# Performance work log

Measured on AMD Instinct MI355X. Metric: run time of the kernel, lower is better.

The kernel has to match this reference:

```python
import jax, jax.numpy as jnp
import numpy as np

N, D_IN, D_OUT, N_CLASSES = 4096, 1024, 256, 64


def setup_inputs() -> dict:
    key = jax.random.key(0)
    k1, k2, k3, k4 = jax.random.split(key, 4)
    x = jax.random.normal(k1, (N, D_IN), dtype=jnp.float32)
    W = jax.random.normal(k2, (D_IN, D_OUT), dtype=jnp.float32) * 0.02
    b = jax.random.normal(k3, (D_OUT,), dtype=jnp.float32) * 0.02
    targets = jax.random.randint(k4, (N,), 0, N_CLASSES, dtype=jnp.int64)
    return {"x": x, "W": W, "b": b, "targets": targets}


def reference(x, W, b, targets):
    # FC projection (activation = 'linear')
    h = jnp.matmul(x, W) + b                      # [N, d]
    # Pairwise euclidean distances D[i, j] = ||h_i - h_j||_2, matching
    # tf.norm(tf.abs(anchor - others), axis=1) in the original per-anchor loop.
    sq = jnp.sum(h * h, axis=1)                   # [N]
    d2 = sq[:, None] + sq[None, :] - 2.0 * jnp.matmul(h, h.T)
    dist = jnp.sqrt(jnp.maximum(d2, 0.0))         # [N, N]
    same = targets[:, None] == targets[None, :]   # class_division mask
    inf = jnp.float32(np.inf)
    # Hardest positive: max distance among same-class (includes self at 0,
    hardest_pos = jnp.max(jnp.where(same, dist, -inf), axis=1)  # [N]
    # Hardest negative: min distance among different-class samples.
    hardest_neg = jnp.min(jnp.where(same, inf, dist), axis=1)   # [N]
    loss = jnp.sum(jnp.log1p(jnp.exp(hardest_pos - hardest_neg)))
    return loss
```

## Files before the change

kernel.cpp:

```cpp
#include <hip/hip_runtime.h>
#include <math.h>

#define NROWS 4096
#define DIN   1024
#define DOUT  256
#define NJB   64
#define NPAIR 528

using bfrag = __attribute__((ext_vector_type(8))) short;
using ffrag = __attribute__((ext_vector_type(4))) float;


static __device__ __forceinline__ unsigned short f2bf(float f) {
    unsigned int u = __float_as_uint(f);
    u = (u + 0x7fffu + ((u >> 16) & 1u)) >> 16;
    return (unsigned short)u;
}
static __device__ __forceinline__ unsigned int pack2(float lo, float hi) {
    return (unsigned int)f2bf(lo) | ((unsigned int)f2bf(hi) << 16);
}

__global__ __launch_bounds__(256) void setup(const float* __restrict__ x,
                                             const float* __restrict__ W,
                                             unsigned short* __restrict__ xs,
                                             unsigned short* __restrict__ Ws,
                                             float* __restrict__ sq,
                                             float* __restrict__ out) {
    const int f  = blockIdx.x * 256 + threadIdx.x;
    {
        const int l  = f & 63;
        const int ks = (f >> 6) & 31;
        const int t  = f >> 11;
        const int row = t * 16 + (l & 15);
        const int k0  = ks * 32 + (l >> 4) * 8;
        const float4 p0 = *(const float4*)&x[(size_t)row * DIN + k0];
        const float4 p1 = *(const float4*)&x[(size_t)row * DIN + k0 + 4];
        uint4 v;
        v.x = pack2(p0.x, p0.y);
        v.y = pack2(p0.z, p0.w);
        v.z = pack2(p1.x, p1.y);
        v.w = pack2(p1.z, p1.w);
        *(uint4*)&xs[(size_t)f * 8] = v;
    }
    if (f < 32768) {
        const int l  = f & 63;
        const int ks = (f >> 6) & 31;
        const int nt = f >> 11;
        const int col = nt * 16 + (l & 15);
        const int k0  = ks * 32 + (l >> 4) * 8;
        float a[8];
#pragma unroll
        for (int j = 0; j < 8; ++j) a[j] = W[(size_t)(k0 + j) * DOUT + col];
        uint4 v;
        v.x = pack2(a[0], a[1]);
        v.y = pack2(a[2], a[3]);
        v.z = pack2(a[4], a[5]);
        v.w = pack2(a[6], a[7]);
        *(uint4*)&Ws[(size_t)f * 8] = v;
    }
    if (f < NROWS) sq[f] = 0.0f;
    if (f == 0) *out = 0.0f;
}

__global__ __launch_bounds__(256) void gemm1_reg(
    const unsigned short* __restrict__ xs, const unsigned short* __restrict__ Ws,
    const float* __restrict__ b,
    unsigned short* __restrict__ hs, float* __restrict__ sq) {
    __shared__ __align__(16) short T[4][16][24];

    const int tid = threadIdx.x;
    const int w   = tid >> 6;
    const int l   = tid & 63;
    const int m16 = l & 15;
    const int q   = l >> 4;
    const int gw  = blockIdx.x * 4 + w;
    const int t   = gw >> 4;
    const int nt  = gw & 15;

    const bfrag* A = (const bfrag*)xs + ((size_t)t * 32) * 64 + l;
    const bfrag* B = (const bfrag*)Ws + ((size_t)nt * 32) * 64 + l;

    ffrag acc = {};
#pragma unroll
    for (int ks = 0; ks < 32; ++ks)
        acc = __builtin_amdgcn_mfma_f32_16x16x32_bf16(A[ks * 64], B[ks * 64], acc, 0, 0, 0);

    const float bc = b[nt * 16 + m16];
    float hv[4];
#pragma unroll
    for (int reg = 0; reg < 4; ++reg) hv[reg] = acc[reg] + bc;

#pragma unroll
    for (int reg = 0; reg < 4; ++reg) {
        float p = hv[reg] * hv[reg];
#pragma unroll
        for (int mask = 1; mask < 16; mask <<= 1) p += __shfl_xor(p, mask);
        if (m16 == 0) atomicAdd(&sq[t * 16 + q * 4 + reg], p);
    }

#pragma unroll
    for (int reg = 0; reg < 4; ++reg)
        T[w][q * 4 + reg][m16] = f2bf(hv[reg]);

    const int ksH  = nt >> 1;
    const int half = nt & 1;
    const int qp   = q - 2 * half;
    if (qp >= 0 && qp < 2) {
        bfrag v = *(const bfrag*)&T[w][m16][qp * 8];
        ((bfrag*)hs)[((size_t)t * 8 + ksH) * 64 + l] = v;
    }
}

__global__ __launch_bounds__(256) void hardest_tri(
    const unsigned short* __restrict__ hs, const float* __restrict__ sq,
    const int* __restrict__ targets,
    float* __restrict__ pmax, float* __restrict__ pmin) {
    const int tid = threadIdx.x;
    const int w   = tid >> 6;
    const int wi  = w & 1, wj = w >> 1;
    const int l   = tid & 63;
    const int m16 = l & 15;
    const int q   = l >> 4;

    const int k = blockIdx.x;
    int bj = (int)((sqrtf(8.0f * (float)k + 1.0f) - 1.0f) * 0.5f);
    while ((bj + 1) * (bj + 2) / 2 <= k) ++bj;
    while (bj * (bj + 1) / 2 > k) --bj;
    const int bi = k - bj * (bj + 1) / 2;
    const bool diag = (bi == bj);

    const int iw = bi * 128 + wi * 64;
    const int jw = bj * 128 + wj * 64;
    const int tA = iw >> 4;
    const int tB = jw >> 4;

    ffrag acc[4][4] = {};

#pragma unroll
    for (int ks = 0; ks < 8; ++ks) {
        bfrag a[4], bb[4];
#pragma unroll
        for (int mi = 0; mi < 4; ++mi)
            a[mi] = *(const bfrag*)&hs[(((size_t)(tA + mi) * 8 + ks) * 64 + l) * 8];
#pragma unroll
        for (int nj = 0; nj < 4; ++nj)
            bb[nj] = *(const bfrag*)&hs[(((size_t)(tB + nj) * 8 + ks) * 64 + l) * 8];
#pragma unroll
        for (int mi = 0; mi < 4; ++mi)
#pragma unroll
            for (int nj = 0; nj < 4; ++nj)
                acc[mi][nj] = __builtin_amdgcn_mfma_f32_16x16x32_bf16(
                    a[mi], bb[nj], acc[mi][nj], 0, 0, 0);
    }

    int   tj[4];
    float svj[4];
#pragma unroll
    for (int nj = 0; nj < 4; ++nj) {
        const int col = jw + nj * 16 + m16;
        tj[nj]  = targets[col];
        svj[nj] = sq[col];
    }

    float cmx[4], cmn[4];
#pragma unroll
    for (int nj = 0; nj < 4; ++nj) { cmx[nj] = -INFINITY; cmn[nj] = INFINITY; }

    const int jblk = bj * 2 + wj;
#pragma unroll
    for (int mi = 0; mi < 4; ++mi)
#pragma unroll
        for (int reg = 0; reg < 4; ++reg) {
            const int row = iw + mi * 16 + q * 4 + reg;
            const int ti  = targets[row];
            const float si = sq[row];
            float mx = -INFINITY, mn = INFINITY;
#pragma unroll
            for (int nj = 0; nj < 4; ++nj) {
                const float g    = acc[mi][nj][reg];
                const float vrow = fmaf(-2.0f, g, svj[nj]);
                const float vcol = fmaf(-2.0f, g, si);
                if (tj[nj] == ti) {
                    mx = fmaxf(mx, vrow);
                    cmx[nj] = fmaxf(cmx[nj], vcol);
                } else {
                    mn = fminf(mn, vrow);
                    cmn[nj] = fminf(cmn[nj], vcol);
                }
            }
#pragma unroll
            for (int mask = 1; mask < 16; mask <<= 1) {
                mx = fmaxf(mx, __shfl_xor(mx, mask));
                mn = fminf(mn, __shfl_xor(mn, mask));
            }
            if (m16 == 0) {
                pmax[(size_t)jblk * NROWS + row] = mx;
                pmin[(size_t)jblk * NROWS + row] = mn;
            }
        }

    if (!diag) {
        const int iblk = bi * 2 + wi;
#pragma unroll
        for (int nj = 0; nj < 4; ++nj) {
            float mx = cmx[nj], mn = cmn[nj];
            mx = fmaxf(mx, __shfl_xor(mx, 16));
            mn = fminf(mn, __shfl_xor(mn, 16));
            mx = fmaxf(mx, __shfl_xor(mx, 32));
            mn = fminf(mn, __shfl_xor(mn, 32));
            if (q == 0) {
                const int col = jw + nj * 16 + m16;
                pmax[(size_t)iblk * NROWS + col] = mx;
                pmin[(size_t)iblk * NROWS + col] = mn;
            }
        }
    }
}

__global__ __launch_bounds__(256) void finalize(const float* __restrict__ sq,
                                                const float* __restrict__ pmax,
                                                const float* __restrict__ pmin,
                                                float* __restrict__ out) {
    __shared__ float wsum[4];
    const int i = blockIdx.x * 256 + threadIdx.x;
    float mp = -INFINITY, mn = INFINITY;
#pragma unroll
    for (int c = 0; c < NJB; ++c) {
        mp = fmaxf(mp, pmax[c * NROWS + i]);
        mn = fminf(mn, pmin[c * NROWS + i]);
    }
    const float si = sq[i];
    const float hp = sqrtf(fmaxf(si + mp, 0.0f));
    const float hn = sqrtf(fmaxf(si + mn, 0.0f));
    const float d  = hp - hn;
    float li = fmaxf(d, 0.0f) + log1pf(expf(-fabsf(d)));
#pragma unroll
    for (int off = 32; off; off >>= 1) li += __shfl_down(li, off);
    const int lane = threadIdx.x & 63, wv = threadIdx.x >> 6;
    if (lane == 0) wsum[wv] = li;
    __syncthreads();
    if (threadIdx.x == 0)
        atomicAdd(out, wsum[0] + wsum[1] + wsum[2] + wsum[3]);
}

extern "C" void kernel_launch(void* const* d_in, const int* in_sizes, int n_in,
                              void* d_out, int out_size, void* d_ws, size_t ws_size,
                              hipStream_t stream) {
    const float* x       = (const float*)d_in[0];
    const float* W       = (const float*)d_in[1];
    const float* b       = (const float*)d_in[2];
    const int*   targets = (const int*)d_in[3];
    float* out = (float*)d_out;

    unsigned short* Ws   = (unsigned short*)d_ws;
    unsigned short* xs   = Ws + DOUT * DIN;
    unsigned short* hs   = xs + (size_t)NROWS * DIN;
    float*          sq   = (float*)(hs + NROWS * DOUT);
    float*          pmax = sq + NROWS;
    float*          pmin = pmax + NJB * NROWS;

    setup<<<(NROWS / 16) * 32 * 64 / 256, 256, 0, stream>>>(x, W, xs, Ws, sq, out);
    gemm1_reg<<<NROWS / 16 * 16 / 4, 256, 0, stream>>>(xs, Ws, b, hs, sq);
    hardest_tri<<<NPAIR, 256, 0, stream>>>(hs, sq, targets, pmax, pmin);
    finalize<<<NROWS / 256, 256, 0, stream>>>(sq, pmax, pmin, out);
}
```

Measured before the change: 121.6 us.

## Fuse fp32-to-bf16 conversion of x into the first GEMM

Removes the pre-pass that converted x to a bf16 fragment layout in workspace. The projection GEMM now loads fp32 x directly, converts it to bf16 in registers, and redistributes the values into the MFMA A-fragment layout with ds_bpermute. The block-to-tile mapping changes so that the 4 waves in a block share one row tile and cover different output column tiles. This drops the 8MB bf16 write and its re-read, and leaves setup handling only W. In exchange, x is read as fp32 several times per row tile, and each k-step adds conversion and cross-lane permute instructions.

```diff
diff --git a/kernel.cpp b/kernel.cpp
--- a/kernel.cpp
+++ b/kernel.cpp
@@ -1,4 +1,5 @@
 #include <hip/hip_runtime.h>
+#include <hip/hip_bf16.h>
 #include <math.h>
 
 #define NROWS 4096
@@ -19,10 +20,14 @@
 static __device__ __forceinline__ unsigned int pack2(float lo, float hi) {
     return (unsigned int)f2bf(lo) | ((unsigned int)f2bf(hi) << 16);
 }
-
-__global__ __launch_bounds__(256) void setup(const float* __restrict__ x,
-                                             const float* __restrict__ W,
-                                             unsigned short* __restrict__ xs,
+static __device__ __forceinline__ int packbf2(float lo, float hi) {
+    float2 t; t.x = lo; t.y = hi;
+    __hip_bfloat162 h = __float22bfloat162_rn(t);
+    union { __hip_bfloat162 h; int i; } u; u.h = h;
+    return u.i;
+}
+
+__global__ __launch_bounds__(256) void setup(const float* __restrict__ W,
                                              unsigned short* __restrict__ Ws,
                                              float* __restrict__ sq,
                                              float* __restrict__ out) {
@@ -30,21 +35,6 @@
     {
         const int l  = f & 63;
         const int ks = (f >> 6) & 31;
-        const int t  = f >> 11;
-        const int row = t * 16 + (l & 15);
-        const int k0  = ks * 32 + (l >> 4) * 8;
-        const float4 p0 = *(const float4*)&x[(size_t)row * DIN + k0];
-        const float4 p1 = *(const float4*)&x[(size_t)row * DIN + k0 + 4];
-        uint4 v;
-        v.x = pack2(p0.x, p0.y);
-        v.y = pack2(p0.z, p0.w);
-        v.z = pack2(p1.x, p1.y);
-        v.w = pack2(p1.z, p1.w);
-        *(uint4*)&xs[(size_t)f * 8] = v;
-    }
-    if (f < 32768) {
-        const int l  = f & 63;
-        const int ks = (f >> 6) & 31;
         const int nt = f >> 11;
         const int col = nt * 16 + (l & 15);
         const int k0  = ks * 32 + (l >> 4) * 8;
@@ -62,8 +52,8 @@
     if (f == 0) *out = 0.0f;
 }
 
-__global__ __launch_bounds__(256) void gemm1_reg(
-    const unsigned short* __restrict__ xs, const unsigned short* __restrict__ Ws,
+__global__ __launch_bounds__(256) void gemm1_fused(
+    const float* __restrict__ x, const unsigned short* __restrict__ Ws,
     const float* __restrict__ b,
     unsigned short* __restrict__ hs, float* __restrict__ sq) {
     __shared__ __align__(16) short T[4][16][24];
@@ -73,17 +63,29 @@
     const int l   = tid & 63;
     const int m16 = l & 15;
     const int q   = l >> 4;
-    const int gw  = blockIdx.x * 4 + w;
-    const int t   = gw >> 4;
-    const int nt  = gw & 15;
-
-    const bfrag* A = (const bfrag*)xs + ((size_t)t * 32) * 64 + l;
+    const int t   = blockIdx.x >> 2;
+    const int nt  = (blockIdx.x & 3) * 4 + w;
+
+    const float* xr = x + (size_t)(t * 16 + (l >> 2)) * DIN + (l & 3) * 8;
+    const int sidx = (((l & 15) * 4) + (l >> 4)) * 4;
     const bfrag* B = (const bfrag*)Ws + ((size_t)nt * 32) * 64 + l;
 
     ffrag acc = {};
 #pragma unroll
-    for (int ks = 0; ks < 32; ++ks)
-        acc = __builtin_amdgcn_mfma_f32_16x16x32_bf16(A[ks * 64], B[ks * 64], acc, 0, 0, 0);
+    for (int ks = 0; ks < 32; ++ks) {
+        const float4 p0 = *(const float4*)(xr + ks * 32);
+        const float4 p1 = *(const float4*)(xr + ks * 32 + 4);
+        const int v0 = packbf2(p0.x, p0.y);
+        const int v1 = packbf2(p0.z, p0.w);
+        const int v2 = packbf2(p1.x, p1.y);
+        const int v3 = packbf2(p1.z, p1.w);
+        union { int i[4]; bfrag f; } u;
+        u.i[0] = __builtin_amdgcn_ds_bpermute(sidx, v0);
+        u.i[1] = __builtin_amdgcn_ds_bpermute(sidx, v1);
+        u.i[2] = __builtin_amdgcn_ds_bpermute(sidx, v2);
+        u.i[3] = __builtin_amdgcn_ds_bpermute(sidx, v3);
+        acc = __builtin_amdgcn_mfma_f32_16x16x32_bf16(u.f, B[ks * 64], acc, 0, 0, 0);
+    }
 
     const float bc = b[nt * 16 + m16];
     float hv[4];
@@ -253,14 +255,13 @@
     float* out = (float*)d_out;
 
     unsigned short* Ws   = (unsigned short*)d_ws;
-    unsigned short* xs   = Ws + DOUT * DIN;
-    unsigned short* hs   = xs + (size_t)NROWS * DIN;
+    unsigned short* hs   = Ws + DOUT * DIN;
     float*          sq   = (float*)(hs + NROWS * DOUT);
     float*          pmax = sq + NROWS;
     float*          pmin = pmax + NJB * NROWS;
 
-    setup<<<(NROWS / 16) * 32 * 64 / 256, 256, 0, stream>>>(x, W, xs, Ws, sq, out);
-    gemm1_reg<<<NROWS / 16 * 16 / 4, 256, 0, stream>>>(xs, Ws, b, hs, sq);
+    setup<<<16 * 32 * 64 / 256, 256, 0, stream>>>(W, Ws, sq, out);
+    gemm1_fused<<<NROWS / 16 * 4, 256, 0, stream>>>(x, Ws, b, hs, sq);
     hardest_tri<<<NPAIR, 256, 0, stream>>>(hs, sq, targets, pmax, pmin);
     finalize<<<NROWS / 256, 256, 0, stream>>>(sq, pmax, pmin, out);
 }
```

After: 127.6 us. +5.0%, slower.
